# Kernel tuning notes

Hardware: AMD Instinct MI355X
Metric: run time of the kernel (lower is better)

Reference implementation:

```python
import jax, jax.numpy as jnp
import numpy as np

# Module constants from init_kwargs
N_X_AXIS = 128
N_Y_AXIS = 128
X_RANGE = (-10.0, 10.0)
Y_RANGE = (-10.0, 10.0)
LOG_L_SCALE = 0.0  # log(1.0), requires_grad=False
N_CTX = 20000


def make_grid():
    # Give_2d_Grid(min_x=x_range[0], max_x=x_range[1], min_y=y_range[1], max_y=y_range[0], flatten=True)
    # -> flattened (G,2) grid; row index i*N_Y_AXIS + j holds [x_i, y_j],
    # with y running from y_range[1] down to y_range[0] (note the swapped args in the source).
    xs = jnp.linspace(X_RANGE[0], X_RANGE[1], N_X_AXIS)
    ys = jnp.linspace(Y_RANGE[1], Y_RANGE[0], N_Y_AXIS)
    gx, gy = jnp.meshgrid(xs, ys, indexing='ij')  # (N_X, N_Y)
    return jnp.stack([gx, gy], axis=-1).reshape(-1, 2)  # (G, 2)


def setup_inputs() -> dict:
    key = jax.random.key(0)
    k1, k2 = jax.random.split(key)
    X = jax.random.normal(k1, (N_CTX, 2), dtype=jnp.float32) * 3.0  # context locations
    Y = jax.random.normal(k2, (N_CTX, 2), dtype=jnp.float32)        # context vectors
    return {"X": X, "Y": Y}


def reference(X, Y):
    # l_scale = exp(clamp(log_l_scale, -5, 5))
    l_scale = jnp.exp(jnp.clip(jnp.asarray(LOG_L_SCALE, X.dtype), -5.0, 5.0))
    grid = make_grid().astype(X.dtype)  # (G, 2)

    # RBF Gram matrix between grid and context points: exp(-||g - x||^2 / (2 l^2))
    # computed via the expanded-square trick to keep it a GEMM + elementwise.
    g2 = jnp.sum(grid * grid, axis=1, keepdims=True)        # (G, 1)
    x2 = jnp.sum(X * X, axis=1, keepdims=True).T            # (1, n)
    d2 = g2 + x2 - 2.0 * (grid @ X.T)                        # (G, n)
    Gram = jnp.exp(-d2 / (2.0 * l_scale * l_scale))          # (G, n)

    # Psi(Y): prepend a ones column -> (n, 3)
    Expand_Y = jnp.concatenate([jnp.ones((Y.shape[0], 1), Y.dtype), Y], axis=1)

    Feature_Map = Gram @ Expand_Y                            # (G, 3)

    # normalize smoothing channels by density channel
    density = Feature_Map[:, :1]
    Norm = jnp.concatenate([density, Feature_Map[:, 1:] / density], axis=1)

    # (G,3) -> (N_X, N_Y, 3) -> permute(2,1,0) -> (3, N_Y, N_X) -> (1, 3, N_Y, N_X)
    out = Norm.reshape(N_X_AXIS, N_Y_AXIS, 3).transpose(2, 1, 0)[None]
    return out
```

## Files before the change

kernel.cpp:

```cpp
#include <hip/hip_runtime.h>


#define NXA 128
#define NG  16384
#define NC  20000
#define KC  32
#define LDA 34
#define NSL 125
#define SLEN 160
#define NCHUNK 5

#define STEP (20.0f / 127.0f)
#define KNEG (-0.72134752044448170368f)

typedef _Float16 v8h  __attribute__((ext_vector_type(8)));
typedef float    v16f __attribute__((ext_vector_type(16)));
typedef float    v4f  __attribute__((ext_vector_type(4)));

__device__ __forceinline__ float fast_exp2(float x) {
    return __builtin_amdgcn_exp2f(x);
}

__global__ __launch_bounds__(256, 1) void k_mfma(const float* __restrict__ X,
                                                 const float* __restrict__ Y,
                                                 _Float16* __restrict__ fm) {
    __shared__ _Float16 Ag[64 * LDA];
    __shared__ _Float16 Bm[384 * LDA];

    const int t     = threadIdx.x;
    const int pp    = blockIdx.x;
    const int slice = blockIdx.y;
    const int n0    = slice * SLEN;

    const int lane = t & 63, wave = t >> 6;
    const int l31 = lane & 31, lh = lane >> 5;
    const int kg = t & 3;
    const int i0 = t >> 2;
    const float gx0 = -10.f + (float)i0 * STEP;
    const float gx1 = -10.f + (float)(i0 + 64) * STEP;
    const float gyj = 10.f - (float)(64 * pp + (t >> 2)) * STEP;

    const float4* Xp = (const float4*)X;
    const float4* Yp = (const float4*)Y;
    const int fb0 = (n0 >> 1) + kg * 4;

    v16f acc[2][3];
#pragma unroll
    for (int jt = 0; jt < 2; ++jt)
#pragma unroll
        for (int m = 0; m < 3; ++m) acc[jt][m] = (v16f)(0.f);

    float4 xf[4], yf[4];
#pragma unroll
    for (int q = 0; q < 4; ++q) { xf[q] = Xp[fb0 + q]; yf[q] = Yp[fb0 + q]; }

#pragma unroll
    for (int m = 0; m < NCHUNK; ++m) {
        float4 xc[4], yc[4];
#pragma unroll
        for (int q = 0; q < 4; ++q) { xc[q] = xf[q]; yc[q] = yf[q]; }

        __syncthreads();

        if (m < NCHUNK - 1) {
            int fb = fb0 + 16 * (m + 1);
#pragma unroll
            for (int q = 0; q < 4; ++q) { xf[q] = Xp[fb + q]; yf[q] = Yp[fb + q]; }
        }

        float xu[8], x1u[8], y0u[8], y1u[8];
#pragma unroll
        for (int q = 0; q < 4; ++q) {
            xu[2 * q]  = xc[q].x;  xu[2 * q + 1]  = xc[q].z;
            x1u[2 * q] = xc[q].y;  x1u[2 * q + 1] = xc[q].w;
            y0u[2 * q] = yc[q].x;  y0u[2 * q + 1] = yc[q].z;
            y1u[2 * q] = yc[q].y;  y1u[2 * q + 1] = yc[q].w;
        }

        {
            v8h e, e1, e2;
#pragma unroll
            for (int u = 0; u < 8; ++u) {
                float dx = gx0 - xu[u];
                float w  = fast_exp2(dx * dx * KNEG);
                e[u]  = (_Float16)w;
                e1[u] = (_Float16)(w * y0u[u]);
                e2[u] = (_Float16)(w * y1u[u]);
            }
            *(v8h*)(Bm + i0 * LDA + kg * 8)         = e;
            *(v8h*)(Bm + (128 + i0) * LDA + kg * 8) = e1;
            *(v8h*)(Bm + (256 + i0) * LDA + kg * 8) = e2;
#pragma unroll
            for (int u = 0; u < 8; ++u) {
                float dx = gx1 - xu[u];
                float w  = fast_exp2(dx * dx * KNEG);
                e[u]  = (_Float16)w;
                e1[u] = (_Float16)(w * y0u[u]);
                e2[u] = (_Float16)(w * y1u[u]);
            }
            *(v8h*)(Bm + (64 + i0) * LDA + kg * 8)  = e;
            *(v8h*)(Bm + (192 + i0) * LDA + kg * 8) = e1;
            *(v8h*)(Bm + (320 + i0) * LDA + kg * 8) = e2;
        }
        {
            v8h a;
#pragma unroll
            for (int u = 0; u < 8; ++u) {
                float dy = gyj - x1u[u];
                a[u] = (_Float16)fast_exp2(dy * dy * KNEG);
            }
            *(v8h*)(Ag + (t >> 2) * LDA + kg * 8) = a;
        }
        __syncthreads();

#pragma unroll
        for (int s = 0; s < 2; ++s) {
            int k = s * 16 + lh * 8;
            v8h af0 = *(const v8h*)(Ag + l31 * LDA + k);
            v8h af1 = *(const v8h*)(Ag + (32 + l31) * LDA + k);
#pragma unroll
            for (int tn = 0; tn < 3; ++tn) {
                int n = wave * 96 + tn * 32 + l31;
                v8h bf = *(const v8h*)(Bm + n * LDA + k);
                acc[0][tn] = __builtin_amdgcn_mfma_f32_32x32x16_f16(af0, bf, acc[0][tn], 0, 0, 0);
                acc[1][tn] = __builtin_amdgcn_mfma_f32_32x32x16_f16(af1, bf, acc[1][tn], 0, 0, 0);
            }
        }
    }

    const size_t cstride = (size_t)NSL * NG;
#pragma unroll
    for (int jt = 0; jt < 2; ++jt)
#pragma unroll
        for (int tn = 0; tn < 3; ++tn) {
            int n = wave * 96 + tn * 32 + l31;
            int c = n >> 7, i = n & 127;
            _Float16* base = fm + (size_t)c * cstride + (size_t)slice * NG + i;
#pragma unroll
            for (int r = 0; r < 16; ++r) {
                int j  = (r & 3) + 8 * (r >> 2) + 4 * lh;
                int gj = 64 * pp + 32 * jt + j;
                base[gj * NXA] = (_Float16)acc[jt][tn][r];
            }
        }
}

__global__ __launch_bounds__(256) void k_reduce_norm(const _Float16* __restrict__ fm,
                                                     float* __restrict__ out) {
    __shared__ v4f sAcc[64][4][7];
    const int t  = threadIdx.x;
    const int q  = t & 3;
    const int sg = t >> 2;
    const int gp = blockIdx.x * 32 + q * 8;
    const size_t cstride = (size_t)NSL * NG;

    v4f a[6];
#pragma unroll
    for (int e = 0; e < 6; ++e) a[e] = (v4f)(0.f);

    const int s0 = sg * 2;
#pragma unroll
    for (int ds = 0; ds < 2; ++ds) {
        int s = s0 + ds;
        if (s < NSL) {
            const _Float16* base = fm + (size_t)s * NG + gp;
#pragma unroll
            for (int ch = 0; ch < 3; ++ch) {
                v8h v = *(const v8h*)(base + ch * cstride);
#pragma unroll
                for (int e = 0; e < 4; ++e) {
                    a[ch * 2][e]     += (float)v[e];
                    a[ch * 2 + 1][e] += (float)v[4 + e];
                }
            }
        }
    }
#pragma unroll
    for (int e = 0; e < 6; ++e) sAcc[sg][q][e] = a[e];

#pragma unroll
    for (int step = 32; step >= 1; step >>= 1) {
        __syncthreads();
        if (t < step * 4) {
            const int qq = t & 3, gg = t >> 2;
#pragma unroll
            for (int e = 0; e < 6; ++e)
                sAcc[gg][qq][e] += sAcc[gg + step][qq][e];
        }
    }
    __syncthreads();
    if (t < 4) {
        v4f Wl = sAcc[0][t][0], Wh = sAcc[0][t][1];
        v4f Pl = sAcc[0][t][2], Ph = sAcc[0][t][3];
        v4f Ql = sAcc[0][t][4], Qh = sAcc[0][t][5];
        v4f il, ih;
#pragma unroll
        for (int e = 0; e < 4; ++e) { il[e] = 1.f / Wl[e]; ih[e] = 1.f / Wh[e]; }
        const int o = blockIdx.x * 32 + t * 8;
        *(v4f*)(out + o)              = Wl;
        *(v4f*)(out + o + 4)          = Wh;
        *(v4f*)(out + NG + o)         = Pl * il;
        *(v4f*)(out + NG + o + 4)     = Ph * ih;
        *(v4f*)(out + 2 * NG + o)     = Ql * il;
        *(v4f*)(out + 2 * NG + o + 4) = Qh * ih;
    }
}

__global__ __launch_bounds__(256) void k_accum_atomic(const float* __restrict__ X,
                                                      const float* __restrict__ Y,
                                                      float* __restrict__ dst,
                                                      int slice_len) {
    __shared__ float As[64 * 64], Bs[64 * 64], Yl[64 * 2];
    const int t = threadIdx.x, tx = t & 15, ty = t >> 4;
    const int pos = blockIdx.x;
    const int tI = (pos >> 1) * 64, tJ = (pos & 1) * 64;
    const int n0 = blockIdx.y * slice_len;
    int nEnd = n0 + slice_len; if (nEnd > NC) nEnd = NC;
    float aw[16], ap[16], aq[16];
#pragma unroll
    for (int k = 0; k < 16; ++k) { aw[k] = ap[k] = aq[k] = 0.f; }
    for (int c0 = n0; c0 < nEnd; c0 += 64) {
        __syncthreads();
#pragma unroll
        for (int k = 0; k < 16; ++k) {
            int l = k * 256 + t, nl = l >> 6, ii = l & 63, n = c0 + nl;
            float a = 0.f, b = 0.f;
            if (n < nEnd) {
                float dx = (-10.f + (float)(tI + ii) * STEP) - X[2 * n];
                float dy = (10.f - (float)(tJ + ii) * STEP) - X[2 * n + 1];
                a = fast_exp2(dx * dx * KNEG);
                b = fast_exp2(dy * dy * KNEG);
            }
            As[nl * 64 + ii] = a; Bs[nl * 64 + ii] = b;
        }
        if (t < 128) { int n = c0 + (t >> 1); Yl[t] = (n < nEnd) ? Y[2 * n + (t & 1)] : 0.f; }
        __syncthreads();
        int cnt = nEnd - c0; if (cnt > 64) cnt = 64;
        for (int n = 0; n < cnt; ++n) {
            const float4 a4 = *(const float4*)(As + n * 64 + tx * 4);
            const float4 b4 = *(const float4*)(Bs + n * 64 + ty * 4);
            float y0 = Yl[2 * n], y1 = Yl[2 * n + 1];
            float av[4] = {a4.x, a4.y, a4.z, a4.w};
            float bv[4] = {b4.x, b4.y, b4.z, b4.w};
#pragma unroll
            for (int di = 0; di < 4; ++di)
#pragma unroll
                for (int dj = 0; dj < 4; ++dj) {
                    int k = di * 4 + dj;
                    float w = av[di] * bv[dj];
                    aw[k] += w; ap[k] = fmaf(w, y0, ap[k]); aq[k] = fmaf(w, y1, aq[k]);
                }
        }
    }
#pragma unroll
    for (int di = 0; di < 4; ++di)
#pragma unroll
        for (int dj = 0; dj < 4; ++dj) {
            int gi = tI + tx * 4 + di, gj = tJ + ty * 4 + dj;
            int o = gj * NXA + gi, k = di * 4 + dj;
            atomicAdd(dst + o, aw[k]);
            atomicAdd(dst + NG + o, ap[k]);
            atomicAdd(dst + 2 * NG + o, aq[k]);
        }
}

__global__ __launch_bounds__(256) void k_norm_inplace(float* __restrict__ out) {
    int t = blockIdx.x * 256 + threadIdx.x;
    if (t >= NG) return;
    float inv = 1.f / out[t];
    out[NG + t] *= inv; out[2 * NG + t] *= inv;
}

extern "C" void kernel_launch(void* const* d_in, const int* in_sizes, int n_in,
                              void* d_out, int out_size, void* d_ws, size_t ws_size,
                              hipStream_t stream) {
    const float* X = (const float*)d_in[0];
    const float* Y = (const float*)d_in[1];
    float* out = (float*)d_out;
    const size_t need = (size_t)NSL * NG * 3 * sizeof(_Float16);
    if (ws_size >= need) {
        _Float16* fm = (_Float16*)d_ws;
        k_mfma<<<dim3(2, NSL), 256, 0, stream>>>(X, Y, fm);
        k_reduce_norm<<<NG / 32, 256, 0, stream>>>(fm, out);
    } else {
        hipMemsetAsync(d_out, 0, (size_t)out_size * sizeof(float), stream);
        k_accum_atomic<<<dim3(4, 64), 256, 0, stream>>>(X, Y, out, (NC + 63) / 64);
        k_norm_inplace<<<(NG + 255) / 256, 256, 0, stream>>>(out);
    }
}
```

Baseline: 72.38 us.

## Fuse MFMA partials and reduction into one kernel with a grid-wide barrier

Merges the partial-feature-map MFMA kernel and the cross-slice reduce/normalize kernel into one launch. After writing its fp16 partials, each block increments a global atomic counter and spins until all 250 blocks arrive, then takes a strided share of the 512 reduction tiles. This removes one kernel launch and the gap between kernels, at the cost of a memset for the counter and a spin barrier that relies on all 250 blocks being resident at once (one block per CU, 256 CUs), with a bounded guard on the spin. Only 250 blocks do the reduction instead of 512, so each runs up to three tile iterations.

```diff
diff --git a/kernel.cpp b/kernel.cpp
--- a/kernel.cpp
+++ b/kernel.cpp
@@ -9,6 +9,8 @@
 #define NSL 125
 #define SLEN 160
 #define NCHUNK 5
+#define NBLK 250
+#define CTR_OFF 12288000
 
 #define STEP (20.0f / 127.0f)
 #define KNEG (-0.72134752044448170368f)
@@ -21,11 +23,14 @@
     return __builtin_amdgcn_exp2f(x);
 }
 
-__global__ __launch_bounds__(256, 1) void k_mfma(const float* __restrict__ X,
-                                                 const float* __restrict__ Y,
-                                                 _Float16* __restrict__ fm) {
+__global__ __launch_bounds__(256, 1) void k_fused(const float* __restrict__ X,
+                                                  const float* __restrict__ Y,
+                                                  _Float16* __restrict__ fm,
+                                                  unsigned* __restrict__ ctr,
+                                                  float* __restrict__ out) {
     __shared__ _Float16 Ag[64 * LDA];
     __shared__ _Float16 Bm[384 * LDA];
+    __shared__ v4f sAcc[64][4][7];
 
     const int t     = threadIdx.x;
     const int pp    = blockIdx.x;
@@ -143,66 +148,76 @@
                 base[gj * NXA] = (_Float16)acc[jt][tn][r];
             }
         }
-}
-
-__global__ __launch_bounds__(256) void k_reduce_norm(const _Float16* __restrict__ fm,
-                                                     float* __restrict__ out) {
-    __shared__ v4f sAcc[64][4][7];
-    const int t  = threadIdx.x;
+
+    __threadfence();
+    __syncthreads();
+    if (t == 0) {
+        __hip_atomic_fetch_add(ctr, 1u, __ATOMIC_ACQ_REL, __HIP_MEMORY_SCOPE_AGENT);
+        unsigned v; unsigned guard = 0;
+        do {
+            v = __hip_atomic_load(ctr, __ATOMIC_ACQUIRE, __HIP_MEMORY_SCOPE_AGENT);
+            if (v >= (unsigned)NBLK) break;
+            __builtin_amdgcn_s_sleep(2);
+        } while (++guard < (1u << 24));
+    }
+    __syncthreads();
+    __threadfence();
+
+    const int b = slice * 2 + pp;
     const int q  = t & 3;
     const int sg = t >> 2;
-    const int gp = blockIdx.x * 32 + q * 8;
-    const size_t cstride = (size_t)NSL * NG;
-
-    v4f a[6];
-#pragma unroll
-    for (int e = 0; e < 6; ++e) a[e] = (v4f)(0.f);
-
-    const int s0 = sg * 2;
-#pragma unroll
-    for (int ds = 0; ds < 2; ++ds) {
-        int s = s0 + ds;
-        if (s < NSL) {
-            const _Float16* base = fm + (size_t)s * NG + gp;
-#pragma unroll
-            for (int ch = 0; ch < 3; ++ch) {
-                v8h v = *(const v8h*)(base + ch * cstride);
-#pragma unroll
-                for (int e = 0; e < 4; ++e) {
-                    a[ch * 2][e]     += (float)v[e];
-                    a[ch * 2 + 1][e] += (float)v[4 + e];
+    for (int tile = b; tile < 512; tile += NBLK) {
+        __syncthreads();
+        const int gp = tile * 32 + q * 8;
+        v4f a[6];
+#pragma unroll
+        for (int e = 0; e < 6; ++e) a[e] = (v4f)(0.f);
+        const int s0 = sg * 2;
+#pragma unroll
+        for (int ds = 0; ds < 2; ++ds) {
+            int s = s0 + ds;
+            if (s < NSL) {
+                const _Float16* base = fm + (size_t)s * NG + gp;
+#pragma unroll
+                for (int ch = 0; ch < 3; ++ch) {
+                    v8h v = *(const v8h*)(base + ch * cstride);
+#pragma unroll
+                    for (int e = 0; e < 4; ++e) {
+                        a[ch * 2][e]     += (float)v[e];
+                        a[ch * 2 + 1][e] += (float)v[4 + e];
+                    }
                 }
             }
         }
-    }
-#pragma unroll
-    for (int e = 0; e < 6; ++e) sAcc[sg][q][e] = a[e];
-
-#pragma unroll
-    for (int step = 32; step >= 1; step >>= 1) {
-        __syncthreads();
-        if (t < step * 4) {
-            const int qq = t & 3, gg = t >> 2;
-#pragma unroll
-            for (int e = 0; e < 6; ++e)
-                sAcc[gg][qq][e] += sAcc[gg + step][qq][e];
-        }
-    }
-    __syncthreads();
-    if (t < 4) {
-        v4f Wl = sAcc[0][t][0], Wh = sAcc[0][t][1];
-        v4f Pl = sAcc[0][t][2], Ph = sAcc[0][t][3];
-        v4f Ql = sAcc[0][t][4], Qh = sAcc[0][t][5];
-        v4f il, ih;
-#pragma unroll
-        for (int e = 0; e < 4; ++e) { il[e] = 1.f / Wl[e]; ih[e] = 1.f / Wh[e]; }
-        const int o = blockIdx.x * 32 + t * 8;
-        *(v4f*)(out + o)              = Wl;
-        *(v4f*)(out + o + 4)          = Wh;
-        *(v4f*)(out + NG + o)         = Pl * il;
-        *(v4f*)(out + NG + o + 4)     = Ph * ih;
-        *(v4f*)(out + 2 * NG + o)     = Ql * il;
-        *(v4f*)(out + 2 * NG + o + 4) = Qh * ih;
+#pragma unroll
+        for (int e = 0; e < 6; ++e) sAcc[sg][q][e] = a[e];
+
+#pragma unroll
+        for (int step = 32; step >= 1; step >>= 1) {
+            __syncthreads();
+            if (t < step * 4) {
+                const int qq = t & 3, gg = t >> 2;
+#pragma unroll
+                for (int e = 0; e < 6; ++e)
+                    sAcc[gg][qq][e] += sAcc[gg + step][qq][e];
+            }
+        }
+        __syncthreads();
+        if (t < 4) {
+            v4f Wl = sAcc[0][t][0], Wh = sAcc[0][t][1];
+            v4f Pl = sAcc[0][t][2], Ph = sAcc[0][t][3];
+            v4f Ql = sAcc[0][t][4], Qh = sAcc[0][t][5];
+            v4f il, ih;
+#pragma unroll
+            for (int e = 0; e < 4; ++e) { il[e] = 1.f / Wl[e]; ih[e] = 1.f / Wh[e]; }
+            const int o = tile * 32 + t * 8;
+            *(v4f*)(out + o)              = Wl;
+            *(v4f*)(out + o + 4)          = Wh;
+            *(v4f*)(out + NG + o)         = Pl * il;
+            *(v4f*)(out + NG + o + 4)     = Ph * ih;
+            *(v4f*)(out + 2 * NG + o)     = Ql * il;
+            *(v4f*)(out + 2 * NG + o + 4) = Qh * ih;
+        }
     }
 }
 
@@ -277,11 +292,12 @@
     const float* X = (const float*)d_in[0];
     const float* Y = (const float*)d_in[1];
     float* out = (float*)d_out;
-    const size_t need = (size_t)NSL * NG * 3 * sizeof(_Float16);
+    const size_t need = (size_t)CTR_OFF + 128;
     if (ws_size >= need) {
         _Float16* fm = (_Float16*)d_ws;
-        k_mfma<<<dim3(2, NSL), 256, 0, stream>>>(X, Y, fm);
-        k_reduce_norm<<<NG / 32, 256, 0, stream>>>(fm, out);
+        unsigned* ctr = (unsigned*)((char*)d_ws + CTR_OFF);
+        hipMemsetAsync(ctr, 0, 4, stream);
+        k_fused<<<dim3(2, NSL), 256, 0, stream>>>(X, Y, fm, ctr, out);
     } else {
         hipMemsetAsync(d_out, 0, (size_t)out_size * sizeof(float), stream);
         k_accum_atomic<<<dim3(4, 64), 256, 0, stream>>>(X, Y, out, (NC + 63) / 64);
```

New measurement: 130.9 us. 80.8% more time.

## Split k_mfma blocks along grid-x halves to double block count

Applied to the files above, without the earlier changes.

Each k_mfma block now handles one 64-wide half of the x-grid instead of all 128 columns, so the launch grows from 2x125 to 4x125 blocks. Each wave holds three accumulators instead of six, shared memory for B shrinks by half, and launch bounds allow two blocks per CU. The aim is to fill more of the CUs with smaller blocks. In exchange, the y-direction exponentials and the X/Y loads are recomputed in twice as many blocks.

```diff
diff --git a/kernel.cpp b/kernel.cpp
--- a/kernel.cpp
+++ b/kernel.cpp
@@ -21,86 +21,75 @@
     return __builtin_amdgcn_exp2f(x);
 }
 
-__global__ __launch_bounds__(256, 1) void k_mfma(const float* __restrict__ X,
+__global__ __launch_bounds__(256, 2) void k_mfma(const float* __restrict__ X,
                                                  const float* __restrict__ Y,
                                                  _Float16* __restrict__ fm) {
     __shared__ _Float16 Ag[64 * LDA];
-    __shared__ _Float16 Bm[384 * LDA];
+    __shared__ _Float16 Bm[192 * LDA];
 
     const int t     = threadIdx.x;
-    const int pp    = blockIdx.x;
+    const int pb    = blockIdx.x;
+    const int pp    = pb >> 1;
+    const int ih    = pb & 1;
     const int slice = blockIdx.y;
     const int n0    = slice * SLEN;
 
     const int lane = t & 63, wave = t >> 6;
     const int l31 = lane & 31, lh = lane >> 5;
+    const int jt = wave >> 1, nh = wave & 1;
     const int kg = t & 3;
-    const int i0 = t >> 2;
-    const float gx0 = -10.f + (float)i0 * STEP;
-    const float gx1 = -10.f + (float)(i0 + 64) * STEP;
-    const float gyj = 10.f - (float)(64 * pp + (t >> 2)) * STEP;
+    const int q  = t >> 2;
+    const float gxq = -10.f + (float)(64 * ih + q) * STEP;
+    const float gyj = 10.f - (float)(64 * pp + q) * STEP;
 
     const float4* Xp = (const float4*)X;
     const float4* Yp = (const float4*)Y;
     const int fb0 = (n0 >> 1) + kg * 4;
 
-    v16f acc[2][3];
-#pragma unroll
-    for (int jt = 0; jt < 2; ++jt)
-#pragma unroll
-        for (int m = 0; m < 3; ++m) acc[jt][m] = (v16f)(0.f);
+    v16f acc[3];
+#pragma unroll
+    for (int m = 0; m < 3; ++m) acc[m] = (v16f)(0.f);
 
     float4 xf[4], yf[4];
 #pragma unroll
-    for (int q = 0; q < 4; ++q) { xf[q] = Xp[fb0 + q]; yf[q] = Yp[fb0 + q]; }
+    for (int qq = 0; qq < 4; ++qq) { xf[qq] = Xp[fb0 + qq]; yf[qq] = Yp[fb0 + qq]; }
 
 #pragma unroll
     for (int m = 0; m < NCHUNK; ++m) {
         float4 xc[4], yc[4];
 #pragma unroll
-        for (int q = 0; q < 4; ++q) { xc[q] = xf[q]; yc[q] = yf[q]; }
+        for (int qq = 0; qq < 4; ++qq) { xc[qq] = xf[qq]; yc[qq] = yf[qq]; }
 
         __syncthreads();
 
         if (m < NCHUNK - 1) {
             int fb = fb0 + 16 * (m + 1);
 #pragma unroll
-            for (int q = 0; q < 4; ++q) { xf[q] = Xp[fb + q]; yf[q] = Yp[fb + q]; }
+            for (int qq = 0; qq < 4; ++qq) { xf[qq] = Xp[fb + qq]; yf[qq] = Yp[fb + qq]; }
         }
 
         float xu[8], x1u[8], y0u[8], y1u[8];
 #pragma unroll
-        for (int q = 0; q < 4; ++q) {
-            xu[2 * q]  = xc[q].x;  xu[2 * q + 1]  = xc[q].z;
-            x1u[2 * q] = xc[q].y;  x1u[2 * q + 1] = xc[q].w;
-            y0u[2 * q] = yc[q].x;  y0u[2 * q + 1] = yc[q].z;
-            y1u[2 * q] = yc[q].y;  y1u[2 * q + 1] = yc[q].w;
+        for (int qq = 0; qq < 4; ++qq) {
+            xu[2 * qq]  = xc[qq].x;  xu[2 * qq + 1]  = xc[qq].z;
+            x1u[2 * qq] = xc[qq].y;  x1u[2 * qq + 1] = xc[qq].w;
+            y0u[2 * qq] = yc[qq].x;  y0u[2 * qq + 1] = yc[qq].z;
+            y1u[2 * qq] = yc[qq].y;  y1u[2 * qq + 1] = yc[qq].w;
         }
 
         {
             v8h e, e1, e2;
 #pragma unroll
             for (int u = 0; u < 8; ++u) {
-                float dx = gx0 - xu[u];
+                float dx = gxq - xu[u];
                 float w  = fast_exp2(dx * dx * KNEG);
                 e[u]  = (_Float16)w;
                 e1[u] = (_Float16)(w * y0u[u]);
                 e2[u] = (_Float16)(w * y1u[u]);
             }
-            *(v8h*)(Bm + i0 * LDA + kg * 8)         = e;
-            *(v8h*)(Bm + (128 + i0) * LDA + kg * 8) = e1;
-            *(v8h*)(Bm + (256 + i0) * LDA + kg * 8) = e2;
-#pragma unroll
-            for (int u = 0; u < 8; ++u) {
-                float dx = gx1 - xu[u];
-                float w  = fast_exp2(dx * dx * KNEG);
-                e[u]  = (_Float16)w;
-                e1[u] = (_Float16)(w * y0u[u]);
-                e2[u] = (_Float16)(w * y1u[u]);
-            }
-            *(v8h*)(Bm + (64 + i0) * LDA + kg * 8)  = e;
-            *(v8h*)(Bm + (192 + i0) * LDA + kg * 8) = e1;
-            *(v8h*)(Bm + (320 + i0) * LDA + kg * 8) = e2;
+            *(v8h*)(Bm + q * LDA + kg * 8)         = e;
+            *(v8h*)(Bm + (64 + q) * LDA + kg * 8)  = e1;
+            *(v8h*)(Bm + (128 + q) * LDA + kg * 8) = e2;
         }
         {
             v8h a;
@@ -109,40 +98,37 @@
                 float dy = gyj - x1u[u];
                 a[u] = (_Float16)fast_exp2(dy * dy * KNEG);
             }
-            *(v8h*)(Ag + (t >> 2) * LDA + kg * 8) = a;
+            *(v8h*)(Ag + q * LDA + kg * 8) = a;
         }
         __syncthreads();
 
 #pragma unroll
         for (int s = 0; s < 2; ++s) {
             int k = s * 16 + lh * 8;
-            v8h af0 = *(const v8h*)(Ag + l31 * LDA + k);
-            v8h af1 = *(const v8h*)(Ag + (32 + l31) * LDA + k);
+            v8h af = *(const v8h*)(Ag + (32 * jt + l31) * LDA + k);
 #pragma unroll
             for (int tn = 0; tn < 3; ++tn) {
-                int n = wave * 96 + tn * 32 + l31;
-                v8h bf = *(const v8h*)(Bm + n * LDA + k);
-                acc[0][tn] = __builtin_amdgcn_mfma_f32_32x32x16_f16(af0, bf, acc[0][tn], 0, 0, 0);
-                acc[1][tn] = __builtin_amdgcn_mfma_f32_32x32x16_f16(af1, bf, acc[1][tn], 0, 0, 0);
+                int np = nh * 96 + tn * 32 + l31;
+                v8h bf = *(const v8h*)(Bm + np * LDA + k);
+                acc[tn] = __builtin_amdgcn_mfma_f32_32x32x16_f16(af, bf, acc[tn], 0, 0, 0);
             }
         }
     }
 
     const size_t cstride = (size_t)NSL * NG;
 #pragma unroll
-    for (int jt = 0; jt < 2; ++jt)
-#pragma unroll
-        for (int tn = 0; tn < 3; ++tn) {
-            int n = wave * 96 + tn * 32 + l31;
-            int c = n >> 7, i = n & 127;
-            _Float16* base = fm + (size_t)c * cstride + (size_t)slice * NG + i;
-#pragma unroll
-            for (int r = 0; r < 16; ++r) {
-                int j  = (r & 3) + 8 * (r >> 2) + 4 * lh;
-                int gj = 64 * pp + 32 * jt + j;
-                base[gj * NXA] = (_Float16)acc[jt][tn][r];
-            }
-        }
+    for (int tn = 0; tn < 3; ++tn) {
+        int np = nh * 96 + tn * 32 + l31;
+        int c  = np >> 6;
+        int i  = 64 * ih + (np & 63);
+        _Float16* base = fm + (size_t)c * cstride + (size_t)slice * NG + i;
+#pragma unroll
+        for (int r = 0; r < 16; ++r) {
+            int j  = (r & 3) + 8 * (r >> 2) + 4 * lh;
+            int gj = 64 * pp + 32 * jt + j;
+            base[gj * NXA] = (_Float16)acc[tn][r];
+        }
+    }
 }
 
 __global__ __launch_bounds__(256) void k_reduce_norm(const _Float16* __restrict__ fm,
@@ -193,16 +179,16 @@
         v4f Wl = sAcc[0][t][0], Wh = sAcc[0][t][1];
         v4f Pl = sAcc[0][t][2], Ph = sAcc[0][t][3];
         v4f Ql = sAcc[0][t][4], Qh = sAcc[0][t][5];
-        v4f il, ih;
-#pragma unroll
-        for (int e = 0; e < 4; ++e) { il[e] = 1.f / Wl[e]; ih[e] = 1.f / Wh[e]; }
+        v4f il, ih2;
+#pragma unroll
+        for (int e = 0; e < 4; ++e) { il[e] = 1.f / Wl[e]; ih2[e] = 1.f / Wh[e]; }
         const int o = blockIdx.x * 32 + t * 8;
         *(v4f*)(out + o)              = Wl;
         *(v4f*)(out + o + 4)          = Wh;
         *(v4f*)(out + NG + o)         = Pl * il;
-        *(v4f*)(out + NG + o + 4)     = Ph * ih;
+        *(v4f*)(out + NG + o + 4)     = Ph * ih2;
         *(v4f*)(out + 2 * NG + o)     = Ql * il;
-        *(v4f*)(out + 2 * NG + o + 4) = Qh * ih;
+        *(v4f*)(out + 2 * NG + o + 4) = Qh * ih2;
     }
 }
 
@@ -280,7 +266,7 @@
     const size_t need = (size_t)NSL * NG * 3 * sizeof(_Float16);
     if (ws_size >= need) {
         _Float16* fm = (_Float16*)d_ws;
-        k_mfma<<<dim3(2, NSL), 256, 0, stream>>>(X, Y, fm);
+        k_mfma<<<dim3(4, NSL), 256, 0, stream>>>(X, Y, fm);
         k_reduce_norm<<<NG / 32, 256, 0, stream>>>(fm, out);
     } else {
         hipMemsetAsync(d_out, 0, (size_t)out_size * sizeof(float), stream);
```

Result: no change. 72.93 us (+0.8%).
